# Performance work log

Hardware: AMD Instinct MI355X
Metric: run time of the kernel (lower is better)

The kernel has to match this reference:

```python
import jax, jax.numpy as jnp
import numpy as np

N, E, B = 50000, 400000, 64
N_INC, E_OUTC, U_INC, G_INC = 64, 64, 32, 64
H1A, H1B = 128, 64           # node_model_mlp1_hidden_sizes
H2 = 256                     # node_model_mlp2_hidden_sizes[0]
DIM_LH, DIM_L, N_OUTC = 128, 32, 64
LN_EPS = 1e-5

def _lin_init(key, din, dout):
    k1, k2 = jax.random.split(key)
    bound = 1.0 / np.sqrt(din)
    W = jax.random.uniform(k1, (din, dout), jnp.float32, -bound, bound)
    b = jax.random.uniform(k2, (dout,), jnp.float32, -bound, bound)
    return W, b

def setup_inputs() -> dict:
    key = jax.random.key(0)
    ks = jax.random.split(key, 16)
    x = jax.random.normal(ks[0], (N, N_INC), jnp.float32)
    edge_index = jax.random.randint(ks[1], (2, E), 0, N, jnp.int64)
    edge_attr = jax.random.normal(ks[2], (E, E_OUTC), jnp.float32)
    u = jax.random.normal(ks[3], (B, U_INC), jnp.float32)
    batch = jnp.sort(jax.random.randint(ks[4], (N,), 0, B, jnp.int64))
    goal = jax.random.normal(ks[5], (N, G_INC), jnp.float32)
    W1, b1 = _lin_init(ks[6], N_INC + E_OUTC, H1A)
    g1, be1 = jnp.ones((H1A,), jnp.float32), jnp.zeros((H1A,), jnp.float32)
    W2, b2 = _lin_init(ks[7], H1A, H1B)
    mlp2_inc = N_INC + H1B + U_INC
    W3, b3 = _lin_init(ks[8], mlp2_inc, H2)
    g3, be3 = jnp.ones((H2,), jnp.float32), jnp.zeros((H2,), jnp.float32)
    W4, b4 = _lin_init(ks[9], H2, DIM_LH)
    g4, be4 = jnp.ones((DIM_LH,), jnp.float32), jnp.zeros((DIM_LH,), jnp.float32)
    Wm, bm = _lin_init(ks[10], DIM_LH, DIM_L)
    Wv, bv = _lin_init(ks[11], DIM_LH, DIM_L)
    Wx, bx = _lin_init(ks[12], DIM_L, N_OUTC)
    return dict(x=x, edge_index=edge_index, edge_attr=edge_attr, u=u, batch=batch,
                goal=goal, W1=W1, b1=b1, g1=g1, be1=be1, W2=W2, b2=b2,
                W3=W3, b3=b3, g3=g3, be3=be3, W4=W4, b4=b4, g4=g4, be4=be4,
                Wm=Wm, bm=bm, Wv=Wv, bv=bv, Wx=Wx, bx=bx)

def _layernorm(h, g, b):
    mu = jnp.mean(h, axis=-1, keepdims=True)
    var = jnp.var(h, axis=-1, keepdims=True)
    return (h - mu) * jax.lax.rsqrt(var + LN_EPS) * g + b

def reference(x, edge_index, edge_attr, u, batch, goal,
              W1, b1, g1, be1, W2, b2,
              W3, b3, g3, be3, W4, b4, g4, be4,
              Wm, bm, Wv, bv, Wx, bx):
    row, col = edge_index[0], edge_index[1]
    # --- edge MLP: gather x[row], concat edge_attr, 2-layer MLP with LN+ReLU
    se = jnp.concatenate([x[row], edge_attr], axis=1)          # [E, n_inc+e_outc]
    h = jax.nn.relu(_layernorm(se @ W1 + b1, g1, be1)) @ W2 + b2  # [E, H1B]
    # --- scatter_mean over destination nodes
    sums = jax.ops.segment_sum(h, col, num_segments=N)          # [N, H1B]
    cnts = jax.ops.segment_sum(jnp.ones((E,), h.dtype), col, num_segments=N)
    aggs = sums / jnp.maximum(cnts, 1.0)[:, None]
    # --- node MLP 2
    z = jnp.concatenate([x, aggs, u[batch]], axis=1)            # [N, mlp2_inc]
    z = jax.nn.relu(_layernorm(z @ W3 + b3, g3, be3))
    z = jax.nn.relu(_layernorm(z @ W4 + b4, g4, be4))           # [N, DIM_LH]
    z_mu = z @ Wm + bm
    z_var = z @ Wv + bv                                         # log-variance
    eps = jax.random.normal(jax.random.key(42), z_mu.shape, z_mu.dtype)
    z_s = z_mu + eps * jnp.exp(0.5 * z_var)                     # reparameterize
    out = z_s @ Wx + bx                                         # [N, n_outc]
    return (out, z_mu, z_var)
```

## Files before the change

### kernel.cpp

```cpp
#include <hip/hip_runtime.h>

#define NN 50000
#define EE 400000
#define NB 49

typedef __attribute__((ext_vector_type(8))) short bf16x8;
typedef __attribute__((ext_vector_type(4))) float f32x4;

__device__ __forceinline__ void fma4(float4& a, float s, const float4& w){
  a.x = fmaf(s, w.x, a.x);
  a.y = fmaf(s, w.y, a.y);
  a.z = fmaf(s, w.z, a.z);
  a.w = fmaf(s, w.w, a.w);
}

__device__ __forceinline__ unsigned short f2bf(float f){
  unsigned u = __float_as_uint(f);
  unsigned r = (u + 0x7fffu + ((u >> 16) & 1u)) >> 16;
  return (unsigned short)r;
}

__device__ __forceinline__ bf16x8 cvt8(float4 lo, float4 hi){
  bf16x8 r;
  r[0]=(short)f2bf(lo.x); r[1]=(short)f2bf(lo.y); r[2]=(short)f2bf(lo.z); r[3]=(short)f2bf(lo.w);
  r[4]=(short)f2bf(hi.x); r[5]=(short)f2bf(hi.y); r[6]=(short)f2bf(hi.z); r[7]=(short)f2bf(hi.w);
  return r;
}

__device__ __forceinline__ unsigned packhl(float v){
  unsigned hi = f2bf(v);
  float fh = __uint_as_float(hi << 16);
  unsigned lo = f2bf(v - fh);
  return (hi << 16) | lo;
}

__device__ __forceinline__ uint4 pack4(float4 v){
  uint4 p;
  p.x = packhl(v.x); p.y = packhl(v.y); p.z = packhl(v.z); p.w = packhl(v.w);
  return p;
}

__device__ __forceinline__ void unpack8(uint4 p0, uint4 p1, bf16x8& hi, bf16x8& lo){
  hi[0]=(short)(p0.x>>16); lo[0]=(short)(p0.x & 0xffffu);
  hi[1]=(short)(p0.y>>16); lo[1]=(short)(p0.y & 0xffffu);
  hi[2]=(short)(p0.z>>16); lo[2]=(short)(p0.z & 0xffffu);
  hi[3]=(short)(p0.w>>16); lo[3]=(short)(p0.w & 0xffffu);
  hi[4]=(short)(p1.x>>16); lo[4]=(short)(p1.x & 0xffffu);
  hi[5]=(short)(p1.y>>16); lo[5]=(short)(p1.y & 0xffffu);
  hi[6]=(short)(p1.z>>16); lo[6]=(short)(p1.z & 0xffffu);
  hi[7]=(short)(p1.w>>16); lo[7]=(short)(p1.w & 0xffffu);
}

__device__ __forceinline__ float blo(unsigned u){ return __uint_as_float(u << 16); }
__device__ __forceinline__ float bhi(unsigned u){ return __uint_as_float(u & 0xffff0000u); }

__device__ __forceinline__ unsigned rotl32(unsigned v, int d){ return (v<<d)|(v>>(32-d)); }

__device__ __forceinline__ float eps_at(unsigned idx){
  const unsigned k0 = 0u, k1 = 42u, k2 = 0x1BD11BDAu ^ 0u ^ 42u;
  unsigned x0 = 0u + k0, x1 = idx + k1;
  const int rotA[4] = {13,15,26,6};
  const int rotB[4] = {17,29,16,24};
  #pragma unroll
  for (int i=0;i<4;i++){ x0 += x1; x1 = rotl32(x1, rotA[i]); x1 ^= x0; }
  x0 += k1; x1 += k2 + 1u;
  #pragma unroll
  for (int i=0;i<4;i++){ x0 += x1; x1 = rotl32(x1, rotB[i]); x1 ^= x0; }
  x0 += k2; x1 += k0 + 2u;
  #pragma unroll
  for (int i=0;i<4;i++){ x0 += x1; x1 = rotl32(x1, rotA[i]); x1 ^= x0; }
  x0 += k0; x1 += k1 + 3u;
  #pragma unroll
  for (int i=0;i<4;i++){ x0 += x1; x1 = rotl32(x1, rotB[i]); x1 ^= x0; }
  x0 += k1; x1 += k2 + 4u;
  #pragma unroll
  for (int i=0;i<4;i++){ x0 += x1; x1 = rotl32(x1, rotA[i]); x1 ^= x0; }
  x0 += k2; x1 += k0 + 5u;
  unsigned bits = x0 ^ x1;
  float f = __uint_as_float((bits >> 9) | 0x3f800000u) - 1.0f;
  const float lo = -0.99999994f;
  float u = f * 2.0f + lo;
  u = fmaxf(u, lo);
  float w = -log1pf(-u*u);
  float p;
  if (w < 5.0f){
    w -= 2.5f;
    p = 2.81022636e-08f;
    p = fmaf(p,w, 3.43273939e-07f);
    p = fmaf(p,w,-3.5233877e-06f);
    p = fmaf(p,w,-4.39150654e-06f);
    p = fmaf(p,w, 0.00021858087f);
    p = fmaf(p,w,-0.00125372503f);
    p = fmaf(p,w,-0.00417768164f);
    p = fmaf(p,w, 0.246640727f);
    p = fmaf(p,w, 1.50140941f);
  } else {
    w = sqrtf(w) - 3.0f;
    p = -0.000200214257f;
    p = fmaf(p,w, 0.000100950558f);
    p = fmaf(p,w, 0.00134934322f);
    p = fmaf(p,w,-0.00367342844f);
    p = fmaf(p,w, 0.00573950773f);
    p = fmaf(p,w,-0.0076224613f);
    p = fmaf(p,w, 0.00943887047f);
    p = fmaf(p,w, 1.00167406f);
    p = fmaf(p,w, 2.83297682f);
  }
  return 1.41421356237f * (p * u);
}

__global__ __launch_bounds__(256) void k_prep_x(const float* __restrict__ x,
                                                unsigned short* __restrict__ xb){
  int t = blockIdx.x*256 + threadIdx.x;
  if (t < NN*64/8){
    const float4* p = (const float4*)(x + t*8);
    bf16x8 v = cvt8(p[0], p[1]);
    *(bf16x8*)(xb + t*8) = v;
  }
}

__global__ __launch_bounds__(256) void k_prep_w(const float* __restrict__ W1,
                                                const float* __restrict__ W2,
                                                unsigned short* __restrict__ W1T,
                                                unsigned short* __restrict__ W2T){
  for (int i = threadIdx.x; i < 128*128; i += 256){
    int n = i >> 7, k = i & 127;
    W1T[i] = f2bf(W1[k*128 + n]);
  }
  for (int i = threadIdx.x; i < 64*128; i += 256){
    int n = i >> 7, k = i & 127;
    W2T[i] = f2bf(W2[k*64 + n]);
  }
}

__global__ __launch_bounds__(256) void k_prep_w34(const float* __restrict__ W3,
                                                  const float* __restrict__ W4,
                                                  unsigned short* __restrict__ W3Th,
                                                  unsigned short* __restrict__ W3Tl,
                                                  unsigned short* __restrict__ W4Th,
                                                  unsigned short* __restrict__ W4Tl){
  int b = blockIdx.x;
  if (b < 256){
    int n = b;
    for (int k = threadIdx.x; k < 160; k += 256){
      float w = W3[k*256 + n];
      unsigned h = f2bf(w);
      float fh = __uint_as_float(h << 16);
      W3Th[n*160 + k] = (unsigned short)h;
      W3Tl[n*160 + k] = f2bf(w - fh);
    }
  } else {
    int n = b - 256;
    int k = threadIdx.x;
    float w = W4[k*128 + n];
    unsigned h = f2bf(w);
    float fh = __uint_as_float(h << 16);
    W4Th[n*256 + k] = (unsigned short)h;
    W4Tl[n*256 + k] = f2bf(w - fh);
  }
}

__global__ __launch_bounds__(256) void k_hist(const int* __restrict__ ei, int* __restrict__ cnt){
  int e = blockIdx.x*256 + threadIdx.x;
  if (e < EE) atomicAdd(&cnt[ei[EE + e]], 1);
}

__global__ __launch_bounds__(256) void k_scan1(const int* __restrict__ cnt,
                                               int* __restrict__ offs,
                                               int* __restrict__ partials){
  __shared__ int sdata[256];
  const int t = threadIdx.x, b = blockIdx.x;
  const int base = b*1024 + t*4;
  int v0 = (base+0 < NN) ? cnt[base+0] : 0;
  int v1 = (base+1 < NN) ? cnt[base+1] : 0;
  int v2 = (base+2 < NN) ? cnt[base+2] : 0;
  int v3 = (base+3 < NN) ? cnt[base+3] : 0;
  int tsum = v0+v1+v2+v3;
  sdata[t] = tsum;
  __syncthreads();
  for (int off=1; off<256; off<<=1){
    int add = (t >= off) ? sdata[t-off] : 0;
    __syncthreads();
    sdata[t] += add;
    __syncthreads();
  }
  int run = sdata[t] - tsum;
  if (base+0 < NN) offs[base+0] = run;  run += v0;
  if (base+1 < NN) offs[base+1] = run;  run += v1;
  if (base+2 < NN) offs[base+2] = run;  run += v2;
  if (base+3 < NN) offs[base+3] = run;
  if (t == 255) partials[b] = sdata[255];
}

__global__ __launch_bounds__(64) void k_scan2(int* __restrict__ partials){
  int l = threadIdx.x;
  int v = (l < NB) ? partials[l] : 0;
  int inc = v;
  #pragma unroll
  for (int off=1; off<64; off<<=1){
    int t = __shfl_up(inc, off);
    if (l >= off) inc += t;
  }
  if (l < NB) partials[l] = inc - v;
}

__global__ __launch_bounds__(256) void k_scan3(int* __restrict__ offs,
                                               const int* __restrict__ partials,
                                               int* __restrict__ cursor){
  const int t = threadIdx.x, b = blockIdx.x;
  const int base = b*1024 + t*4;
  int add = partials[b];
  #pragma unroll
  for (int k=0;k<4;k++){
    int i = base + k;
    if (i < NN){ int o = offs[i] + add; offs[i] = o; cursor[i] = o; }
  }
}

__global__ __launch_bounds__(256) void k_fill(const int* __restrict__ ei,
                                              int* __restrict__ cursor,
                                              int* __restrict__ epos){
  int e = blockIdx.x*256 + threadIdx.x;
  if (e < EE){
    int c = ei[EE + e];
    epos[e] = atomicAdd(&cursor[c], 1);
  }
}

#define H1STR 132
__global__ __launch_bounds__(256, 4) void k_edge(const int* __restrict__ ei,
    const float* __restrict__ ea,
    const unsigned short* __restrict__ xb,
    const unsigned short* __restrict__ W1T, const float* __restrict__ b1,
    const float* __restrict__ g1, const float* __restrict__ be1,
    const unsigned short* __restrict__ W2T, const float* __restrict__ b2,
    const int* __restrict__ epos,
    unsigned short* __restrict__ h_ws){
  __shared__ __align__(16) float h1[64*H1STR];
  __shared__ int rows_l[64];
  __shared__ int slot_l[64];
  const int tid  = threadIdx.x;
  const int base = blockIdx.x * 64;
  const int wv   = tid >> 6;
  const int lane = tid & 63;
  const int quad = lane >> 4;
  const int l16  = lane & 15;
  if (tid < 64) rows_l[tid] = ei[base + tid];
  if (tid >= 128 && tid < 192) slot_l[tid-128] = epos[base + tid - 128];
  __syncthreads();
  {
    int rw[4];
    #pragma unroll
    for (int m=0;m<4;m++) rw[m] = rows_l[m*16 + l16];
    f32x4 acc[4][2];
    #pragma unroll
    for (int m=0;m<4;m++){ acc[m][0] = (f32x4){0.f,0.f,0.f,0.f}; acc[m][1] = (f32x4){0.f,0.f,0.f,0.f}; }
    #pragma unroll
    for (int ks=0; ks<4; ks++){
      bf16x8 af[4];
      if (ks < 2){
        #pragma unroll
        for (int m=0;m<4;m++)
          af[m] = *(const bf16x8*)(xb + (size_t)rw[m]*64 + ks*32 + quad*8);
      } else {
        #pragma unroll
        for (int m=0;m<4;m++){
          const float* p = ea + (size_t)(base + m*16 + l16)*64 + (ks-2)*32 + quad*8;
          af[m] = cvt8(*(const float4*)p, *(const float4*)(p+4));
        }
      }
      bf16x8 bf0 = *(const bf16x8*)(W1T + (size_t)((2*wv+0)*16 + l16)*128 + ks*32 + quad*8);
      bf16x8 bf1 = *(const bf16x8*)(W1T + (size_t)((2*wv+1)*16 + l16)*128 + ks*32 + quad*8);
      #pragma unroll
      for (int m=0;m<4;m++){
        acc[m][0] = __builtin_amdgcn_mfma_f32_16x16x32_bf16(af[m], bf0, acc[m][0], 0, 0, 0);
        acc[m][1] = __builtin_amdgcn_mfma_f32_16x16x32_bf16(af[m], bf1, acc[m][1], 0, 0, 0);
      }
    }
    #pragma unroll
    for (int nl=0; nl<2; nl++){
      float b1c = b1[(2*wv+nl)*16 + l16];
      #pragma unroll
      for (int m=0;m<4;m++){
        #pragma unroll
        for (int r=0;r<4;r++)
          h1[(m*16 + quad*4 + r)*H1STR + (2*wv+nl)*16 + l16] = acc[m][nl][r] + b1c;
      }
    }
  }
  __syncthreads();
  {
    const float gA = g1[lane], gB = g1[lane+64];
    const float bA = be1[lane], bB = be1[lane+64];
    for (int r = wv*16; r < wv*16 + 16; ++r){
      float a = h1[r*H1STR + lane];
      float b = h1[r*H1STR + 64 + lane];
      float s = a + b, ss = fmaf(a,a,b*b);
      #pragma unroll
      for (int off=32; off; off>>=1){
        s  += __shfl_xor(s, off);
        ss += __shfl_xor(ss, off);
      }
      float mean = s * (1.0f/128.0f);
      float var  = ss * (1.0f/128.0f) - mean*mean;
      float inv = rsqrtf(var + 1e-5f);
      h1[r*H1STR + lane]      = fmaxf(fmaf((a-mean)*inv, gA, bA), 0.f);
      h1[r*H1STR + 64 + lane] = fmaxf(fmaf((b-mean)*inv, gB, bB), 0.f);
    }
  }
  __syncthreads();
  {
    f32x4 acc2[4];
    #pragma unroll
    for (int m=0;m<4;m++) acc2[m] = (f32x4){0.f,0.f,0.f,0.f};
    #pragma unroll
    for (int ks=0; ks<4; ks++){
      bf16x8 bfr = *(const bf16x8*)(W2T + (size_t)(wv*16 + l16)*128 + ks*32 + quad*8);
      #pragma unroll
      for (int m=0;m<4;m++){
        const float* p = h1 + (m*16 + l16)*H1STR + ks*32 + quad*8;
        bf16x8 af = cvt8(*(const float4*)p, *(const float4*)(p+4));
        acc2[m] = __builtin_amdgcn_mfma_f32_16x16x32_bf16(af, bfr, acc2[m], 0, 0, 0);
      }
    }
    float b2c = b2[wv*16 + l16];
    #pragma unroll
    for (int m=0;m<4;m++){
      #pragma unroll
      for (int r=0;r<4;r++)
        h_ws[(size_t)slot_l[m*16 + quad*4 + r]*64 + wv*16 + l16] = f2bf(acc2[m][r] + b2c);
    }
  }
}

__global__ __launch_bounds__(256, 8) void k_agg(const float* __restrict__ x,
    const float* __restrict__ u, const int* __restrict__ batch,
    const unsigned short* __restrict__ h_ws, const int* __restrict__ cnt,
    const int* __restrict__ offs, unsigned* __restrict__ zg){
  int t = blockIdx.x*256 + threadIdx.x;
  int n = t >> 3, p = t & 7;
  if (n >= NN) return;
  unsigned* zr = zg + (size_t)n*160;
  {
    const float4* xp = (const float4*)(x + (size_t)n*64 + p*8);
    *(uint4*)(zr + p*8)     = pack4(xp[0]);
    *(uint4*)(zr + p*8 + 4) = pack4(xp[1]);
  }
  {
    const float4* up = (const float4*)(u + (size_t)batch[n]*32 + p*4);
    *(uint4*)(zr + 128 + p*4) = pack4(up[0]);
  }
  float a0=0.f,a1=0.f,a2=0.f,a3=0.f,a4=0.f,a5=0.f,a6=0.f,a7=0.f;
  int deg = cnt[n];
  const unsigned short* hp = h_ws + (size_t)offs[n]*64 + p*8;
  int j = 0;
  for (; j + 4 <= deg; j += 4){
    uint4 v0 = *(const uint4*)(hp);
    uint4 v1 = *(const uint4*)(hp + 64);
    uint4 v2 = *(const uint4*)(hp + 128);
    uint4 v3 = *(const uint4*)(hp + 192);
    hp += 256;
    a0 += blo(v0.x); a1 += bhi(v0.x); a2 += blo(v0.y); a3 += bhi(v0.y);
    a4 += blo(v0.z); a5 += bhi(v0.z); a6 += blo(v0.w); a7 += bhi(v0.w);
    a0 += blo(v1.x); a1 += bhi(v1.x); a2 += blo(v1.y); a3 += bhi(v1.y);
    a4 += blo(v1.z); a5 += bhi(v1.z); a6 += blo(v1.w); a7 += bhi(v1.w);
    a0 += blo(v2.x); a1 += bhi(v2.x); a2 += blo(v2.y); a3 += bhi(v2.y);
    a4 += blo(v2.z); a5 += bhi(v2.z); a6 += blo(v2.w); a7 += bhi(v2.w);
    a0 += blo(v3.x); a1 += bhi(v3.x); a2 += blo(v3.y); a3 += bhi(v3.y);
    a4 += blo(v3.z); a5 += bhi(v3.z); a6 += blo(v3.w); a7 += bhi(v3.w);
  }
  for (; j < deg; ++j){
    uint4 v = *(const uint4*)(hp);
    hp += 64;
    a0 += blo(v.x); a1 += bhi(v.x); a2 += blo(v.y); a3 += bhi(v.y);
    a4 += blo(v.z); a5 += bhi(v.z); a6 += blo(v.w); a7 += bhi(v.w);
  }
  float rc = 1.0f / fmaxf((float)deg, 1.0f);
  *(uint4*)(zr + 64 + p*8)     = pack4(make_float4(a0*rc, a1*rc, a2*rc, a3*rc));
  *(uint4*)(zr + 64 + p*8 + 4) = pack4(make_float4(a4*rc, a5*rc, a6*rc, a7*rc));
}

#define T2STR 132
#define ZSSTR 36
#define H3STR 260
__global__ __launch_bounds__(256, 2) void k_node(const unsigned* __restrict__ zg,
    const unsigned short* __restrict__ W3Th, const unsigned short* __restrict__ W3Tl,
    const float* __restrict__ b3,
    const float* __restrict__ g3, const float* __restrict__ be3,
    const unsigned short* __restrict__ W4Th, const unsigned short* __restrict__ W4Tl,
    const float* __restrict__ b4,
    const float* __restrict__ g4, const float* __restrict__ be4,
    const float* __restrict__ Wm, const float* __restrict__ bm,
    const float* __restrict__ Wv, const float* __restrict__ bv,
    const float* __restrict__ Wx, const float* __restrict__ bx,
    float* __restrict__ out){
  __shared__ __align__(16) char arena[64*H3STR*4];
  float*    h3f = (float*)arena;
  unsigned* h3p = (unsigned*)arena;
  float*    t2S = (float*)arena;
  float*    hmS = (float*)(arena + 33792);
  float*    zsS = (float*)(arena + 50176);

  const int tid = threadIdx.x;
  const int base = blockIdx.x * 64;
  const int wv   = tid >> 6;
  const int lane = tid & 63;
  const int quad = lane >> 4;
  const int l16  = lane & 15;

  {
    f32x4 acc[4][4];
    #pragma unroll
    for (int m=0;m<4;m++)
      #pragma unroll
      for (int i=0;i<4;i++) acc[m][i] = (f32x4){0.f,0.f,0.f,0.f};
    #pragma unroll
    for (int ks=0; ks<5; ks++){
      bf16x8 ah[4], al[4];
      #pragma unroll
      for (int m=0;m<4;m++){
        const unsigned* az = zg + (size_t)(base + m*16 + l16)*160 + ks*32 + quad*8;
        uint4 p0 = *(const uint4*)az;
        uint4 p1 = *(const uint4*)(az + 4);
        unpack8(p0, p1, ah[m], al[m]);
      }
      #pragma unroll
      for (int i=0;i<4;i++){
        int nt = wv*4 + i;
        bf16x8 bh = *(const bf16x8*)(W3Th + (size_t)(nt*16 + l16)*160 + ks*32 + quad*8);
        bf16x8 bl = *(const bf16x8*)(W3Tl + (size_t)(nt*16 + l16)*160 + ks*32 + quad*8);
        #pragma unroll
        for (int m=0;m<4;m++){
          acc[m][i] = __builtin_amdgcn_mfma_f32_16x16x32_bf16(ah[m], bh, acc[m][i], 0, 0, 0);
          acc[m][i] = __builtin_amdgcn_mfma_f32_16x16x32_bf16(al[m], bh, acc[m][i], 0, 0, 0);
          acc[m][i] = __builtin_amdgcn_mfma_f32_16x16x32_bf16(ah[m], bl, acc[m][i], 0, 0, 0);
        }
      }
    }
    #pragma unroll
    for (int i=0;i<4;i++){
      int nt = wv*4 + i;
      float bc = b3[nt*16 + l16];
      #pragma unroll
      for (int m=0;m<4;m++)
        #pragma unroll
        for (int r=0;r<4;r++)
          h3f[(m*16 + quad*4 + r)*H3STR + nt*16 + l16] = acc[m][i][r] + bc;
    }
  }
  __syncthreads();
  {
    float4 gg  = *(const float4*)(g3 + lane*4);
    float4 bet = *(const float4*)(be3 + lane*4);
    #pragma unroll
    for (int r=0;r<16;r++){
      int row = wv*16 + r;
      float4 v = *(const float4*)(h3f + row*H3STR + lane*4);
      float s  = v.x + v.y + v.z + v.w;
      float ss = fmaf(v.x,v.x, fmaf(v.y,v.y, fmaf(v.z,v.z, v.w*v.w)));
      #pragma unroll
      for (int off=32; off; off>>=1){ s += __shfl_xor(s,off); ss += __shfl_xor(ss,off); }
      float mean = s * (1.0f/256.0f);
      float inv  = rsqrtf(ss*(1.0f/256.0f) - mean*mean + 1e-5f);
      float4 o;
      o.x = fmaxf(fmaf((v.x-mean)*inv, gg.x, bet.x), 0.f);
      o.y = fmaxf(fmaf((v.y-mean)*inv, gg.y, bet.y), 0.f);
      o.z = fmaxf(fmaf((v.z-mean)*inv, gg.z, bet.z), 0.f);
      o.w = fmaxf(fmaf((v.w-mean)*inv, gg.w, bet.w), 0.f);
      *(uint4*)(h3p + row*H3STR + lane*4) = pack4(o);
    }
  }
  __syncthreads();
  {
    f32x4 acc2[4][2];
    #pragma unroll
    for (int m=0;m<4;m++){ acc2[m][0] = (f32x4){0.f,0.f,0.f,0.f}; acc2[m][1] = (f32x4){0.f,0.f,0.f,0.f}; }
    #pragma unroll
    for (int ks=0; ks<8; ks++){
      bf16x8 ah[4], al[4];
      #pragma unroll
      for (int m=0;m<4;m++){
        const unsigned* ap = h3p + (m*16 + l16)*H3STR + ks*32 + quad*8;
        uint4 p0 = *(const uint4*)ap;
        uint4 p1 = *(const uint4*)(ap + 4);
        unpack8(p0, p1, ah[m], al[m]);
      }
      #pragma unroll
      for (int i=0;i<2;i++){
        int nt = wv*2 + i;
        bf16x8 bh = *(const bf16x8*)(W4Th + (size_t)(nt*16 + l16)*256 + ks*32 + quad*8);
        bf16x8 bl = *(const bf16x8*)(W4Tl + (size_t)(nt*16 + l16)*256 + ks*32 + quad*8);
        #pragma unroll
        for (int m=0;m<4;m++){
          acc2[m][i] = __builtin_amdgcn_mfma_f32_16x16x32_bf16(ah[m], bh, acc2[m][i], 0, 0, 0);
          acc2[m][i] = __builtin_amdgcn_mfma_f32_16x16x32_bf16(al[m], bh, acc2[m][i], 0, 0, 0);
          acc2[m][i] = __builtin_amdgcn_mfma_f32_16x16x32_bf16(ah[m], bl, acc2[m][i], 0, 0, 0);
        }
      }
    }
    __syncthreads();
    #pragma unroll
    for (int i=0;i<2;i++){
      int nt = wv*2 + i;
      float bc = b4[nt*16 + l16];
      #pragma unroll
      for (int m=0;m<4;m++)
        #pragma unroll
        for (int r=0;r<4;r++)
          t2S[(m*16 + quad*4 + r)*T2STR + nt*16 + l16] = acc2[m][i][r] + bc;
    }
  }
  __syncthreads();
  {
    const int jq = tid & 31, rb = tid >> 5;
    float4 gg  = *(const float4*)(g4 + 4*jq);
    float4 bet = *(const float4*)(be4 + 4*jq);
    #pragma unroll
    for (int r=0;r<8;r++){
      int row = rb*8 + r;
      float4 v = *(const float4*)(t2S + row*T2STR + 4*jq);
      float s  = v.x + v.y + v.z + v.w;
      float ss = fmaf(v.x,v.x, fmaf(v.y,v.y, fmaf(v.z,v.z, v.w*v.w)));
      #pragma unroll
      for (int off=16; off; off>>=1){ s += __shfl_xor(s,off); ss += __shfl_xor(ss,off); }
      float mean = s * (1.0f/128.0f);
      float inv  = rsqrtf(ss*(1.0f/128.0f) - mean*mean + 1e-5f);
      float4 o;
      o.x = fmaxf(fmaf((v.x-mean)*inv, gg.x, bet.x), 0.f);
      o.y = fmaxf(fmaf((v.y-mean)*inv, gg.y, bet.y), 0.f);
      o.z = fmaxf(fmaf((v.z-mean)*inv, gg.z, bet.z), 0.f);
      o.w = fmaxf(fmaf((v.w-mean)*inv, gg.w, bet.w), 0.f);
      *(float4*)(t2S + row*T2STR + 4*jq) = o;
    }
  }
  __syncthreads();
  {
    const int jq = tid & 15, rb = tid >> 4;
    const float* Wp = (jq < 8) ? Wm : Wv;
    const int cq = (jq & 7) * 4;
    float4 acc[4];
    #pragma unroll
    for (int r=0;r<4;r++) acc[r] = make_float4(0.f,0.f,0.f,0.f);
    #pragma unroll 2
    for (int k=0;k<128;k+=4){
      float4 w0 = *(const float4*)(Wp + (k+0)*32 + cq);
      float4 w1 = *(const float4*)(Wp + (k+1)*32 + cq);
      float4 w2 = *(const float4*)(Wp + (k+2)*32 + cq);
      float4 w3 = *(const float4*)(Wp + (k+3)*32 + cq);
      #pragma unroll
      for (int r=0;r<4;r++){
        float4 z = *(const float4*)(t2S + (rb*4+r)*T2STR + k);
        fma4(acc[r], z.x, w0); fma4(acc[r], z.y, w1);
        fma4(acc[r], z.z, w2); fma4(acc[r], z.w, w3);
      }
    }
    const float* bp = (jq < 8) ? bm : bv;
    float4 bb = *(const float4*)(bp + cq);
    const long long sec = (jq < 8) ? (long long)NN*64 : ((long long)NN*64 + (long long)NN*32);
    #pragma unroll
    for (int r=0;r<4;r++){
      float4 v = acc[r];
      v.x += bb.x; v.y += bb.y; v.z += bb.z; v.w += bb.w;
      int rr = rb*4 + r;
      *(float4*)(hmS + rr*64 + ((jq<8)?0:32) + cq) = v;
      int n = base + rr;
      if (n < NN) *(float4*)(out + sec + (long long)n*32 + cq) = v;
    }
  }
  __syncthreads();
  #pragma unroll
  for (int i=0;i<8;i++){
    int l = tid + 256*i;
    int r = l >> 5, jj = l & 31;
    float mu = hmS[r*64 + jj];
    float lv = hmS[r*64 + 32 + jj];
    unsigned idx = (unsigned)((base + r)*32 + jj);
    float e = eps_at(idx);
    zsS[r*ZSSTR + jj] = fmaf(e, expf(0.5f*lv), mu);
  }
  __syncthreads();
  {
    const int jq = tid & 15, rb = tid >> 4;
    float4 acc[4];
    #pragma unroll
    for (int r=0;r<4;r++) acc[r] = make_float4(0.f,0.f,0.f,0.f);
    #pragma unroll
    for (int k=0;k<32;k+=4){
      float4 w0 = *(const float4*)(Wx + (k+0)*64 + 4*jq);
      float4 w1 = *(const float4*)(Wx + (k+1)*64 + 4*jq);
      float4 w2 = *(const float4*)(Wx + (k+2)*64 + 4*jq);
      float4 w3 = *(const float4*)(Wx + (k+3)*64 + 4*jq);
      #pragma unroll
      for (int r=0;r<4;r++){
        float4 z = *(const float4*)(zsS + (rb*4+r)*ZSSTR + k);
        fma4(acc[r], z.x, w0); fma4(acc[r], z.y, w1);
        fma4(acc[r], z.z, w2); fma4(acc[r], z.w, w3);
      }
    }
    float4 bb = *(const float4*)(bx + 4*jq);
    #pragma unroll
    for (int r=0;r<4;r++){
      int n = base + rb*4 + r;
      if (n < NN){
        float4 v = acc[r];
        v.x += bb.x; v.y += bb.y; v.z += bb.z; v.w += bb.w;
        *(float4*)(out + (long long)n*64 + 4*jq) = v;
      }
    }
  }
}

extern "C" void kernel_launch(void* const* d_in, const int* in_sizes, int n_in,
                              void* d_out, int out_size, void* d_ws, size_t ws_size,
                              hipStream_t stream) {
  const float* x     = (const float*)d_in[0];
  const int*   ei    = (const int*)d_in[1];
  const float* ea    = (const float*)d_in[2];
  const float* u     = (const float*)d_in[3];
  const int*   batch = (const int*)d_in[4];
  const float* W1 = (const float*)d_in[6];
  const float* b1 = (const float*)d_in[7];
  const float* g1 = (const float*)d_in[8];
  const float* be1= (const float*)d_in[9];
  const float* W2 = (const float*)d_in[10];
  const float* b2 = (const float*)d_in[11];
  const float* W3 = (const float*)d_in[12];
  const float* b3 = (const float*)d_in[13];
  const float* g3 = (const float*)d_in[14];
  const float* be3= (const float*)d_in[15];
  const float* W4 = (const float*)d_in[16];
  const float* b4 = (const float*)d_in[17];
  const float* g4 = (const float*)d_in[18];
  const float* be4= (const float*)d_in[19];
  const float* Wm = (const float*)d_in[20];
  const float* bm = (const float*)d_in[21];
  const float* Wv = (const float*)d_in[22];
  const float* bv = (const float*)d_in[23];
  const float* Wx = (const float*)d_in[24];
  const float* bx = (const float*)d_in[25];

  char* W = (char*)d_ws;
  size_t off = 0;
  unsigned short* h_ws = (unsigned short*)(W + off); off += (size_t)EE*64*2;
  int* cnt      = (int*)(W + off);  off += (size_t)NN*4;
  int* offs     = (int*)(W + off);  off += (size_t)NN*4;
  int* cursor   = (int*)(W + off);  off += (size_t)NN*4;
  int* epos     = (int*)(W + off);  off += (size_t)EE*4;
  int* partials = (int*)(W + off);  off += 256;
  unsigned short* xb  = (unsigned short*)(W + off); off += (size_t)NN*64*2;
  unsigned short* W1T = (unsigned short*)(W + off); off += 128*128*2;
  unsigned short* W2T = (unsigned short*)(W + off); off += 64*128*2;
  unsigned short* W3Th = (unsigned short*)(W + off); off += 256*160*2;
  unsigned short* W3Tl = (unsigned short*)(W + off); off += 256*160*2;
  unsigned short* W4Th = (unsigned short*)(W + off); off += 128*256*2;
  unsigned short* W4Tl = (unsigned short*)(W + off); off += 128*256*2;
  off = (off + 255) & ~(size_t)255;
  unsigned* zg = (unsigned*)(W + off); off += (size_t)(NN + 64)*160*4;
  float* out = (float*)d_out;

  hipMemsetAsync(cnt, 0, (size_t)NN*sizeof(int), stream);

  k_prep_x<<<(NN*64/8 + 255)/256, 256, 0, stream>>>(x, xb);
  k_prep_w<<<1, 256, 0, stream>>>(W1, W2, W1T, W2T);
  k_prep_w34<<<384, 256, 0, stream>>>(W3, W4, W3Th, W3Tl, W4Th, W4Tl);
  k_hist <<<(EE+255)/256, 256, 0, stream>>>(ei, cnt);
  k_scan1<<<NB, 256, 0, stream>>>(cnt, offs, partials);
  k_scan2<<<1, 64, 0, stream>>>(partials);
  k_scan3<<<NB, 256, 0, stream>>>(offs, partials, cursor);
  k_fill <<<(EE+255)/256, 256, 0, stream>>>(ei, cursor, epos);

  k_edge<<<EE/64, 256, 0, stream>>>(ei, ea, xb, W1T, b1, g1, be1, W2T, b2, epos, h_ws);
  k_agg <<<(NN*8 + 255)/256, 256, 0, stream>>>(x, u, batch, h_ws, cnt, offs, zg);
  k_node<<<(NN+63)/64, 256, 0, stream>>>(zg,
                                         W3Th, W3Tl, b3, g3, be3,
                                         W4Th, W4Tl, b4, g4, be4,
                                         Wm,bm, Wv,bv, Wx,bx, out);
}
```

Baseline: 495.0 us.

## Use packed bf16 convert instructions and split hi/lo node input planes

Replaces the software bf16 rounding helpers with the hardware v_cvt_pk_bf16_f32 instruction and byte-permute unpacking. The interleaved hi/lo packed node input buffer becomes two separate bf16 planes, so k_node loads MFMA fragments directly without unpacking. The edge kernel also reads row indices straight from global memory and drops one shared-memory staging step and barrier. The main risk is the inline-asm conversion, whose rounding may differ slightly from the manual round-to-nearest-even code.

```diff
diff --git a/kernel.cpp b/kernel.cpp
--- a/kernel.cpp
+++ b/kernel.cpp
@@ -20,35 +20,49 @@
   return (unsigned short)r;
 }
 
-__device__ __forceinline__ bf16x8 cvt8(float4 lo, float4 hi){
-  bf16x8 r;
-  r[0]=(short)f2bf(lo.x); r[1]=(short)f2bf(lo.y); r[2]=(short)f2bf(lo.z); r[3]=(short)f2bf(lo.w);
-  r[4]=(short)f2bf(hi.x); r[5]=(short)f2bf(hi.y); r[6]=(short)f2bf(hi.z); r[7]=(short)f2bf(hi.w);
+__device__ __forceinline__ unsigned cvtpk(float lo, float hi){
+  unsigned r;
+  asm("v_cvt_pk_bf16_f32 %0, %1, %2" : "=v"(r) : "v"(lo), "v"(hi));
   return r;
 }
 
-__device__ __forceinline__ unsigned packhl(float v){
-  unsigned hi = f2bf(v);
-  float fh = __uint_as_float(hi << 16);
-  unsigned lo = f2bf(v - fh);
-  return (hi << 16) | lo;
-}
-
-__device__ __forceinline__ uint4 pack4(float4 v){
+__device__ __forceinline__ bf16x8 cvt8pk(float4 a, float4 b){
+  union { unsigned u[4]; bf16x8 v; } r;
+  r.u[0] = cvtpk(a.x, a.y);
+  r.u[1] = cvtpk(a.z, a.w);
+  r.u[2] = cvtpk(b.x, b.y);
+  r.u[3] = cvtpk(b.z, b.w);
+  return r.v;
+}
+
+__device__ __forceinline__ uint4 pack4pk(float4 v){
+  unsigned h01 = cvtpk(v.x, v.y);
+  unsigned h23 = cvtpk(v.z, v.w);
+  float f0 = __uint_as_float(h01 << 16);
+  float f1 = __uint_as_float(h01 & 0xffff0000u);
+  float f2 = __uint_as_float(h23 << 16);
+  float f3 = __uint_as_float(h23 & 0xffff0000u);
+  unsigned l01 = cvtpk(v.x - f0, v.y - f1);
+  unsigned l23 = cvtpk(v.z - f2, v.w - f3);
   uint4 p;
-  p.x = packhl(v.x); p.y = packhl(v.y); p.z = packhl(v.z); p.w = packhl(v.w);
+  p.x = __builtin_amdgcn_perm(h01, l01, 0x05040100u);
+  p.y = __builtin_amdgcn_perm(h01, l01, 0x07060302u);
+  p.z = __builtin_amdgcn_perm(h23, l23, 0x05040100u);
+  p.w = __builtin_amdgcn_perm(h23, l23, 0x07060302u);
   return p;
 }
 
-__device__ __forceinline__ void unpack8(uint4 p0, uint4 p1, bf16x8& hi, bf16x8& lo){
-  hi[0]=(short)(p0.x>>16); lo[0]=(short)(p0.x & 0xffffu);
-  hi[1]=(short)(p0.y>>16); lo[1]=(short)(p0.y & 0xffffu);
-  hi[2]=(short)(p0.z>>16); lo[2]=(short)(p0.z & 0xffffu);
-  hi[3]=(short)(p0.w>>16); lo[3]=(short)(p0.w & 0xffffu);
-  hi[4]=(short)(p1.x>>16); lo[4]=(short)(p1.x & 0xffffu);
-  hi[5]=(short)(p1.y>>16); lo[5]=(short)(p1.y & 0xffffu);
-  hi[6]=(short)(p1.z>>16); lo[6]=(short)(p1.z & 0xffffu);
-  hi[7]=(short)(p1.w>>16); lo[7]=(short)(p1.w & 0xffffu);
+__device__ __forceinline__ void unpack8pk(uint4 p0, uint4 p1, bf16x8& hi, bf16x8& lo){
+  union { unsigned u[4]; bf16x8 v; } H, L;
+  H.u[0] = __builtin_amdgcn_perm(p0.y, p0.x, 0x07060302u);
+  L.u[0] = __builtin_amdgcn_perm(p0.y, p0.x, 0x05040100u);
+  H.u[1] = __builtin_amdgcn_perm(p0.w, p0.z, 0x07060302u);
+  L.u[1] = __builtin_amdgcn_perm(p0.w, p0.z, 0x05040100u);
+  H.u[2] = __builtin_amdgcn_perm(p1.y, p1.x, 0x07060302u);
+  L.u[2] = __builtin_amdgcn_perm(p1.y, p1.x, 0x05040100u);
+  H.u[3] = __builtin_amdgcn_perm(p1.w, p1.z, 0x07060302u);
+  L.u[3] = __builtin_amdgcn_perm(p1.w, p1.z, 0x05040100u);
+  hi = H.v; lo = L.v;
 }
 
 __device__ __forceinline__ float blo(unsigned u){ return __uint_as_float(u << 16); }
@@ -114,7 +128,7 @@
   int t = blockIdx.x*256 + threadIdx.x;
   if (t < NN*64/8){
     const float4* p = (const float4*)(x + t*8);
-    bf16x8 v = cvt8(p[0], p[1]);
+    bf16x8 v = cvt8pk(p[0], p[1]);
     *(bf16x8*)(xb + t*8) = v;
   }
 }
@@ -237,7 +251,6 @@
     const int* __restrict__ epos,
     unsigned short* __restrict__ h_ws){
   __shared__ __align__(16) float h1[64*H1STR];
-  __shared__ int rows_l[64];
   __shared__ int slot_l[64];
   const int tid  = threadIdx.x;
   const int base = blockIdx.x * 64;
@@ -245,13 +258,11 @@
   const int lane = tid & 63;
   const int quad = lane >> 4;
   const int l16  = lane & 15;
-  if (tid < 64) rows_l[tid] = ei[base + tid];
   if (tid >= 128 && tid < 192) slot_l[tid-128] = epos[base + tid - 128];
-  __syncthreads();
   {
     int rw[4];
     #pragma unroll
-    for (int m=0;m<4;m++) rw[m] = rows_l[m*16 + l16];
+    for (int m=0;m<4;m++) rw[m] = ei[base + m*16 + l16];
     f32x4 acc[4][2];
     #pragma unroll
     for (int m=0;m<4;m++){ acc[m][0] = (f32x4){0.f,0.f,0.f,0.f}; acc[m][1] = (f32x4){0.f,0.f,0.f,0.f}; }
@@ -266,7 +277,7 @@
         #pragma unroll
         for (int m=0;m<4;m++){
           const float* p = ea + (size_t)(base + m*16 + l16)*64 + (ks-2)*32 + quad*8;
-          af[m] = cvt8(*(const float4*)p, *(const float4*)(p+4));
+          af[m] = cvt8pk(*(const float4*)p, *(const float4*)(p+4));
         }
       }
       bf16x8 bf0 = *(const bf16x8*)(W1T + (size_t)((2*wv+0)*16 + l16)*128 + ks*32 + quad*8);
@@ -319,7 +330,7 @@
       #pragma unroll
       for (int m=0;m<4;m++){
         const float* p = h1 + (m*16 + l16)*H1STR + ks*32 + quad*8;
-        bf16x8 af = cvt8(*(const float4*)p, *(const float4*)(p+4));
+        bf16x8 af = cvt8pk(*(const float4*)p, *(const float4*)(p+4));
         acc2[m] = __builtin_amdgcn_mfma_f32_16x16x32_bf16(af, bfr, acc2[m], 0, 0, 0);
       }
     }
@@ -336,19 +347,33 @@
 __global__ __launch_bounds__(256, 8) void k_agg(const float* __restrict__ x,
     const float* __restrict__ u, const int* __restrict__ batch,
     const unsigned short* __restrict__ h_ws, const int* __restrict__ cnt,
-    const int* __restrict__ offs, unsigned* __restrict__ zg){
+    const int* __restrict__ offs,
+    unsigned short* __restrict__ zgh, unsigned short* __restrict__ zgl){
   int t = blockIdx.x*256 + threadIdx.x;
   int n = t >> 3, p = t & 7;
   if (n >= NN) return;
-  unsigned* zr = zg + (size_t)n*160;
+  const size_t rb = (size_t)n*160;
   {
     const float4* xp = (const float4*)(x + (size_t)n*64 + p*8);
-    *(uint4*)(zr + p*8)     = pack4(xp[0]);
-    *(uint4*)(zr + p*8 + 4) = pack4(xp[1]);
+    float4 a = xp[0], b = xp[1];
+    unsigned h0 = cvtpk(a.x,a.y), h1v = cvtpk(a.z,a.w), h2 = cvtpk(b.x,b.y), h3v = cvtpk(b.z,b.w);
+    *(uint4*)(zgh + rb + p*8) = make_uint4(h0,h1v,h2,h3v);
+    float4 fh0 = make_float4(__uint_as_float(h0<<16), __uint_as_float(h0&0xffff0000u),
+                             __uint_as_float(h1v<<16), __uint_as_float(h1v&0xffff0000u));
+    float4 fh1 = make_float4(__uint_as_float(h2<<16), __uint_as_float(h2&0xffff0000u),
+                             __uint_as_float(h3v<<16), __uint_as_float(h3v&0xffff0000u));
+    unsigned l0 = cvtpk(a.x-fh0.x, a.y-fh0.y), l1 = cvtpk(a.z-fh0.z, a.w-fh0.w);
+    unsigned l2 = cvtpk(b.x-fh1.x, b.y-fh1.y), l3 = cvtpk(b.z-fh1.z, b.w-fh1.w);
+    *(uint4*)(zgl + rb + p*8) = make_uint4(l0,l1,l2,l3);
   }
   {
     const float4* up = (const float4*)(u + (size_t)batch[n]*32 + p*4);
-    *(uint4*)(zr + 128 + p*4) = pack4(up[0]);
+    float4 a = up[0];
+    unsigned h0 = cvtpk(a.x,a.y), h1v = cvtpk(a.z,a.w);
+    *(uint2*)(zgh + rb + 128 + p*4) = make_uint2(h0,h1v);
+    unsigned l0 = cvtpk(a.x-__uint_as_float(h0<<16), a.y-__uint_as_float(h0&0xffff0000u));
+    unsigned l1 = cvtpk(a.z-__uint_as_float(h1v<<16), a.w-__uint_as_float(h1v&0xffff0000u));
+    *(uint2*)(zgl + rb + 128 + p*4) = make_uint2(l0,l1);
   }
   float a0=0.f,a1=0.f,a2=0.f,a3=0.f,a4=0.f,a5=0.f,a6=0.f,a7=0.f;
   int deg = cnt[n];
@@ -376,14 +401,22 @@
     a4 += blo(v.z); a5 += bhi(v.z); a6 += blo(v.w); a7 += bhi(v.w);
   }
   float rc = 1.0f / fmaxf((float)deg, 1.0f);
-  *(uint4*)(zr + 64 + p*8)     = pack4(make_float4(a0*rc, a1*rc, a2*rc, a3*rc));
-  *(uint4*)(zr + 64 + p*8 + 4) = pack4(make_float4(a4*rc, a5*rc, a6*rc, a7*rc));
+  float4 A = make_float4(a0*rc, a1*rc, a2*rc, a3*rc);
+  float4 B = make_float4(a4*rc, a5*rc, a6*rc, a7*rc);
+  unsigned h0 = cvtpk(A.x,A.y), h1v = cvtpk(A.z,A.w), h2 = cvtpk(B.x,B.y), h3v = cvtpk(B.z,B.w);
+  *(uint4*)(zgh + rb + 64 + p*8) = make_uint4(h0,h1v,h2,h3v);
+  unsigned l0 = cvtpk(A.x-__uint_as_float(h0<<16),  A.y-__uint_as_float(h0&0xffff0000u));
+  unsigned l1 = cvtpk(A.z-__uint_as_float(h1v<<16), A.w-__uint_as_float(h1v&0xffff0000u));
+  unsigned l2 = cvtpk(B.x-__uint_as_float(h2<<16),  B.y-__uint_as_float(h2&0xffff0000u));
+  unsigned l3 = cvtpk(B.z-__uint_as_float(h3v<<16), B.w-__uint_as_float(h3v&0xffff0000u));
+  *(uint4*)(zgl + rb + 64 + p*8) = make_uint4(l0,l1,l2,l3);
 }
 
 #define T2STR 132
 #define ZSSTR 36
 #define H3STR 260
-__global__ __launch_bounds__(256, 2) void k_node(const unsigned* __restrict__ zg,
+__global__ __launch_bounds__(256, 2) void k_node(
+    const unsigned short* __restrict__ zgh, const unsigned short* __restrict__ zgl,
     const unsigned short* __restrict__ W3Th, const unsigned short* __restrict__ W3Tl,
     const float* __restrict__ b3,
     const float* __restrict__ g3, const float* __restrict__ be3,
@@ -419,10 +452,9 @@
       bf16x8 ah[4], al[4];
       #pragma unroll
       for (int m=0;m<4;m++){
-        const unsigned* az = zg + (size_t)(base + m*16 + l16)*160 + ks*32 + quad*8;
-        uint4 p0 = *(const uint4*)az;
-        uint4 p1 = *(const uint4*)(az + 4);
-        unpack8(p0, p1, ah[m], al[m]);
+        size_t o = (size_t)(base + m*16 + l16)*160 + ks*32 + quad*8;
+        ah[m] = *(const bf16x8*)(zgh + o);
+        al[m] = *(const bf16x8*)(zgl + o);
       }
       #pragma unroll
       for (int i=0;i<4;i++){
@@ -467,7 +499,7 @@
       o.y = fmaxf(fmaf((v.y-mean)*inv, gg.y, bet.y), 0.f);
       o.z = fmaxf(fmaf((v.z-mean)*inv, gg.z, bet.z), 0.f);
       o.w = fmaxf(fmaf((v.w-mean)*inv, gg.w, bet.w), 0.f);
-      *(uint4*)(h3p + row*H3STR + lane*4) = pack4(o);
+      *(uint4*)(h3p + row*H3STR + lane*4) = pack4pk(o);
     }
   }
   __syncthreads();
@@ -483,7 +515,7 @@
         const unsigned* ap = h3p + (m*16 + l16)*H3STR + ks*32 + quad*8;
         uint4 p0 = *(const uint4*)ap;
         uint4 p1 = *(const uint4*)(ap + 4);
-        unpack8(p0, p1, ah[m], al[m]);
+        unpack8pk(p0, p1, ah[m], al[m]);
       }
       #pragma unroll
       for (int i=0;i<2;i++){
@@ -655,7 +687,8 @@
   unsigned short* W4Th = (unsigned short*)(W + off); off += 128*256*2;
   unsigned short* W4Tl = (unsigned short*)(W + off); off += 128*256*2;
   off = (off + 255) & ~(size_t)255;
-  unsigned* zg = (unsigned*)(W + off); off += (size_t)(NN + 64)*160*4;
+  unsigned short* zgh = (unsigned short*)(W + off); off += (size_t)(NN + 64)*160*2;
+  unsigned short* zgl = (unsigned short*)(W + off); off += (size_t)(NN + 64)*160*2;
   float* out = (float*)d_out;
 
   hipMemsetAsync(cnt, 0, (size_t)NN*sizeof(int), stream);
@@ -670,8 +703,8 @@
   k_fill <<<(EE+255)/256, 256, 0, stream>>>(ei, cursor, epos);
 
   k_edge<<<EE/64, 256, 0, stream>>>(ei, ea, xb, W1T, b1, g1, be1, W2T, b2, epos, h_ws);
-  k_agg <<<(NN*8 + 255)/256, 256, 0, stream>>>(x, u, batch, h_ws, cnt, offs, zg);
-  k_node<<<(NN+63)/64, 256, 0, stream>>>(zg,
+  k_agg <<<(NN*8 + 255)/256, 256, 0, stream>>>(x, u, batch, h_ws, cnt, offs, zgh, zgl);
+  k_node<<<(NN+63)/64, 256, 0, stream>>>(zgh, zgl,
                                          W3Th, W3Tl, b3, g3, be3,
                                          W4Th, W4Tl, b4, g4, be4,
                                          Wm,bm, Wv,bv, Wx,bx, out);
```

After: 484.0 us. 2.2% less time.
